# Kernel tuning notes

Hardware: AMD Instinct MI355X
Metric: run time of the kernel (lower is better)

The kernel has to match this reference:

```python
import jax, jax.numpy as jnp
import numpy as np

N_WIRES = 9
N_QRAM_LAYERS = 3
N_QCLS_LAYERS = 5

X = jnp.array([[0, 1], [1, 0]], dtype=jnp.complex64)
CNOT = jnp.array([[1, 0, 0, 0], [0, 1, 0, 0], [0, 0, 0, 1], [0, 0, 1, 0]], dtype=jnp.complex64)


def _rx(t):
    c = jnp.cos(t / 2)
    s = jnp.sin(t / 2)
    # works for scalar t -> (2,2) or batched t [B] -> (B,2,2)
    return jnp.stack([jnp.stack([c + 0j, -1j * s], -1), jnp.stack([-1j * s, c + 0j], -1)], -2)


def _ry(t):
    c = jnp.cos(t / 2)
    s = jnp.sin(t / 2)
    return jnp.stack([jnp.stack([c, -s], -1), jnp.stack([s, c], -1)], -2).astype(jnp.complex64)


def _rz(t):
    e = jnp.exp(-0.5j * t)
    f = jnp.exp(0.5j * t)
    z = jnp.zeros_like(e)
    return jnp.stack([jnp.stack([e, z], -1), jnp.stack([z, f], -1)], -2)


def _rot(phi, theta, omega):
    # PennyLane Rot(phi, theta, omega) = RZ(omega) @ RY(theta) @ RZ(phi)
    return _rz(omega) @ _ry(theta) @ _rz(phi)


def _crz(t):
    e = jnp.exp(-0.5j * t)
    f = jnp.exp(0.5j * t)
    one = jnp.ones((), e.dtype)
    return jnp.diag(jnp.stack([one, one, e, f]))


def _crx(t):
    return jnp.eye(4, dtype=jnp.complex64).at[2:, 2:].set(_rx(t))


def apply_1q(state, U, w):
    # state: [B] + (2,)*N_WIRES ; wire w -> axis 1+w
    s = jnp.moveaxis(state, 1 + w, -1)
    if U.ndim == 3:  # per-sample gate (embedding)
        s = jnp.einsum('bij,b...j->b...i', U, s)
    else:
        s = jnp.einsum('ij,...j->...i', U, s)
    return jnp.moveaxis(s, -1, 1 + w)


def apply_2q(state, U, c, t):
    s = jnp.moveaxis(state, (1 + c, 1 + t), (-2, -1))
    shp = s.shape
    s = s.reshape(shp[:-2] + (4,))
    s = jnp.einsum('ij,...j->...i', U, s)
    return jnp.moveaxis(s.reshape(shp), (-2, -1), (1 + c, 1 + t))


def embed(state, adds):
    # AngleEmbedding: RX(adds[:, i]) on wire i
    for i in range(N_WIRES):
        state = apply_1q(state, _rx(adds[:, i]), i)
    return state


def entangle_block(state, p):
    # p: [36] = 4 params per wire-pair step
    j = 0
    for i in range(N_WIRES):
        ip = (i + 1) % N_WIRES
        state = apply_1q(state, _ry(p[j]), i)
        state = apply_1q(state, _ry(p[j + 1]), ip)
        state = apply_2q(state, CNOT, i, ip)
        state = apply_2q(state, _crz(p[j + 2]), i, ip)
        state = apply_1q(state, X, ip)
        state = apply_2q(state, _crx(p[j + 3]), i, ip)
        j += 4
    return state


def sel_layer(state, w, r):
    # one StronglyEntanglingLayers layer: Rot on each wire, then CNOT ring of range r
    for i in range(N_WIRES):
        state = apply_1q(state, _rot(w[i, 0], w[i, 1], w[i, 2]), i)
    for i in range(N_WIRES):
        state = apply_2q(state, CNOT, i, (i + r) % N_WIRES)
    return state


def circuit(adds, params, weights, params2):
    B = adds.shape[0]
    state = jnp.zeros((B,) + (2,) * N_WIRES, jnp.complex64)
    state = state.at[(slice(None),) + (0,) * N_WIRES].set(1.0)
    state = embed(state, adds)
    for l in range(N_QRAM_LAYERS):
        state = entangle_block(state, params[l * 36:(l + 1) * 36])
    for l in range(N_QRAM_LAYERS):
        r = (l % (N_WIRES - 1)) + 1  # PennyLane default ranges
        state = sel_layer(state, weights[l], r)
    for l in range(N_QCLS_LAYERS):
        state = entangle_block(state, params2[l * 36:(l + 1) * 36])
    probs = jnp.abs(state) ** 2
    p = probs.reshape(B, 2, -1).sum(-1)  # marginal over wire 0
    return p[:, 0] - p[:, 1]  # <PauliZ(0)>


def setup_inputs() -> dict:
    key = jax.random.key(0)
    k1, k2, k3, k4 = jax.random.split(key, 4)
    B = 8192
    return {
        'adds': jax.random.normal(k1, (B, N_WIRES), dtype=jnp.float32),
        'params': jax.random.normal(k2, (N_QRAM_LAYERS * 36,), dtype=jnp.float32),
        'weights': jax.random.normal(k3, (N_QRAM_LAYERS, N_WIRES, N_QRAM_LAYERS), dtype=jnp.float32),
        'params2': jax.random.normal(k4, (N_QCLS_LAYERS * 36,), dtype=jnp.float32),
    }


def reference(adds, params, weights, params2):
    return circuit(adds, params, weights, params2)
```

## Files before the change

kernel.cpp:

```cpp
#include <hip/hip_runtime.h>

#define NQ 9
#define NS 512
#define M2 1024
#define NSIMB 256

#define COEF_ROT_BASE (72*32)
#define COEF_R3_BASE  (COEF_ROT_BASE + 27*8)
#define COEF_FLOATS   (COEF_R3_BASE + 3*128)

typedef __attribute__((ext_vector_type(8))) short bf16x8;
typedef __attribute__((ext_vector_type(4))) float f32x4;

__device__ inline unsigned short f2bf(float f){
  unsigned int u = __float_as_uint(f);
  u += 0x7fffu + ((u >> 16) & 1u);
  return (unsigned short)(u >> 16);
}


template<int LM>
__device__ inline float lxor(float v){
  if constexpr (LM == 1)
    return __int_as_float(__builtin_amdgcn_mov_dpp(__float_as_int(v), 0xB1, 0xF, 0xF, true));
  else if constexpr (LM == 2)
    return __int_as_float(__builtin_amdgcn_mov_dpp(__float_as_int(v), 0x4E, 0xF, 0xF, true));
  else if constexpr (LM == 3)
    return __int_as_float(__builtin_amdgcn_mov_dpp(__float_as_int(v), 0x1B, 0xF, 0xF, true));
  else if constexpr (LM < 32)
    return __int_as_float(__builtin_amdgcn_ds_swizzle(__float_as_int(v), (LM<<10)|0x1F));
  else
    return __shfl_xor(v, LM);
}

template<int M>
__device__ inline float lx(float v){
  if constexpr ((M & 63) == 0) return v;
  else return lxor<(M & 63)>(v);
}

template<int M>
__device__ inline void getp(const float (&ox)[4], const float (&oy)[4],
                            const float2 (&pv)[4], int r, float& qx, float& qy){
  constexpr int MR = (M >> 6) & 3;
  float vx, vy;
  if constexpr ((M & 0x100) != 0){ vx = pv[r^MR].x; vy = pv[r^MR].y; }
  else                           { vx = ox[r^MR];   vy = oy[r^MR];   }
  qx = lx<M>(vx); qy = lx<M>(vy);
}

__device__ inline void xwave(const float (&ax)[4], const float (&ay)[4],
                             int wvb, int lane, float2* xb, float2 (&pv)[4]){
  #pragma unroll
  for (int r = 0; r < 4; ++r) xb[(wvb*4+r)*64 + lane] = make_float2(ax[r], ay[r]);
  __syncthreads();
  #pragma unroll
  for (int r = 0; r < 4; ++r) pv[r] = xb[((wvb^1)*4+r)*64 + lane];
}

template<int CM,int TM>
__device__ inline void stepQ(float (&ax)[4], float (&ay)[4], int wvb, int lane,
                             float2* xb, const float* g){
  constexpr bool HX = ((CM | TM) & 0x100) != 0;
  float2 pv[4];
  if constexpr (HX) xwave(ax, ay, wvb, lane, xb, pv);
  float ox[4], oy[4];
  #pragma unroll
  for (int r = 0; r < 4; ++r){ ox[r] = ax[r]; oy[r] = ay[r]; }
  #pragma unroll
  for (int r = 0; r < 4; ++r){
    float tx,ty,cx,cy,bx,by;
    getp<TM>(ox, oy, pv, r, tx, ty);
    getp<CM>(ox, oy, pv, r, cx, cy);
    getp<(CM^TM)>(ox, oy, pv, r, bx, by);
    int i = (wvb << 8) | (r << 6) | lane;
    int p = ((i & CM) ? 2 : 0) | ((i & TM) ? 1 : 0);
    float4 hx = *(const float4*)(g + p*4);
    float4 hy = *(const float4*)(g + 16 + p*4);
    ax[r] = hx.x*ox[r]-hy.x*oy[r] + hx.y*tx-hy.y*ty + hx.z*cx-hy.z*cy + hx.w*bx-hy.w*by;
    ay[r] = hx.x*oy[r]+hy.x*ox[r] + hx.y*ty+hy.y*tx + hx.z*cy+hy.z*cx + hx.w*by+hy.w*bx;
  }
}

template<int I = 0>
__device__ inline void ent_blkQ(float (&ax)[4], float (&ay)[4], int wvb, int lane,
                                float2* ebA, float2* ebB, const float* S){
  if constexpr      (I == 0) stepQ<0x100,0x080>(ax, ay, wvb, lane, ebA, S);
  else if constexpr (I == 8) stepQ<0x001,0x100>(ax, ay, wvb, lane, ebB, S + 256);
  else                       stepQ<(0x100>>I),(0x080>>I)>(ax, ay, wvb, lane, ebA, S + I*32);
  if constexpr (I < 8) ent_blkQ<I+1>(ax, ay, wvb, lane, ebA, ebB, S);
}

__device__ inline void rot3Q(float (&ax)[4], float (&ay)[4], int wvb, int lane,
                             float2* xb, const float* Mt){
  float2 pv[4];
  xwave(ax, ay, wvb, lane, xb, pv);
  bool w1 = (wvb != 0);
  float l0x[4],l0y[4],l1x[4],l1y[4];
  #pragma unroll
  for (int r = 0; r < 4; ++r){
    l0x[r] = w1 ? pv[r].x : ax[r];  l0y[r] = w1 ? pv[r].y : ay[r];
    l1x[r] = w1 ? ax[r]   : pv[r].x; l1y[r] = w1 ? ay[r]   : pv[r].y;
  }
  #pragma unroll
  for (int r = 0; r < 4; ++r){
    const float4* row = (const float4*)(Mt + ((wvb<<2)|r)*16);
    float4 m0 = row[0], m1 = row[1], m2 = row[2], m3 = row[3];
    float nx, ny;
    nx  = m0.x*l0x[0]-m0.y*l0y[0];  ny  = m0.x*l0y[0]+m0.y*l0x[0];
    nx += m0.z*l0x[1]-m0.w*l0y[1];  ny += m0.z*l0y[1]+m0.w*l0x[1];
    nx += m1.x*l0x[2]-m1.y*l0y[2];  ny += m1.x*l0y[2]+m1.y*l0x[2];
    nx += m1.z*l0x[3]-m1.w*l0y[3];  ny += m1.z*l0y[3]+m1.w*l0x[3];
    nx += m2.x*l1x[0]-m2.y*l1y[0];  ny += m2.x*l1y[0]+m2.y*l1x[0];
    nx += m2.z*l1x[1]-m2.w*l1y[1];  ny += m2.z*l1y[1]+m2.w*l1x[1];
    nx += m3.x*l1x[2]-m3.y*l1y[2];  ny += m3.x*l1y[2]+m3.y*l1x[2];
    nx += m3.z*l1x[3]-m3.w*l1y[3];  ny += m3.z*l1y[3]+m3.w*l1x[3];
    ax[r] = nx; ay[r] = ny;
  }
}

template<int LM>
__device__ inline void rotQ(float (&ax)[4], float (&ay)[4], int lane, const float* u){
  float4 uu = *(const float4*)(u + ((lane & LM) ? 4 : 0));
  #pragma unroll
  for (int r = 0; r < 4; ++r){
    float px = lxor<LM>(ax[r]), py = lxor<LM>(ay[r]);
    float nx = uu.x*ax[r]-uu.y*ay[r] + uu.z*px-uu.w*py;
    float ny = uu.x*ay[r]+uu.y*ax[r] + uu.z*py+uu.w*px;
    ax[r] = nx; ay[r] = ny;
  }
}

template<int I = 3>
__device__ inline void sel_rotsQ(float (&ax)[4], float (&ay)[4], int lane, const float* ub){
  rotQ<(1<<(8-I))>(ax, ay, lane, ub + I*8);
  if constexpr (I < 8) sel_rotsQ<I+1>(ax, ay, lane, ub);
}

template<int TR>
__device__ inline void cn_wr(float (&ax)[4], float (&ay)[4], int wvb){
  if (wvb){
    #pragma unroll
    for (int r = 0; r < 4; ++r) if (!(r & TR)){
      float t = ax[r]; ax[r] = ax[r|TR]; ax[r|TR] = t;
      t = ay[r]; ay[r] = ay[r|TR]; ay[r|TR] = t;
    }
  }
}
template<int TL>
__device__ inline void cn_wl(float (&ax)[4], float (&ay)[4], int wvb){
  if (wvb){
    #pragma unroll
    for (int r = 0; r < 4; ++r){ ax[r] = lxor<TL>(ax[r]); ay[r] = lxor<TL>(ay[r]); }
  }
}
template<int CR,int TR>
__device__ inline void cn_rr(float (&ax)[4], float (&ay)[4]){
  #pragma unroll
  for (int r = 0; r < 4; ++r) if ((r & CR) && !(r & TR)){
    float t = ax[r]; ax[r] = ax[r|TR]; ax[r|TR] = t;
    t = ay[r]; ay[r] = ay[r|TR]; ay[r|TR] = t;
  }
}
template<int CR,int TL>
__device__ inline void cn_rl(float (&ax)[4], float (&ay)[4]){
  #pragma unroll
  for (int r = 0; r < 4; ++r) if (r & CR){ ax[r] = lxor<TL>(ax[r]); ay[r] = lxor<TL>(ay[r]); }
}
template<int CL,int TR>
__device__ inline void cn_lr(float (&ax)[4], float (&ay)[4], int lane){
  bool c = (lane & CL) != 0;
  #pragma unroll
  for (int r = 0; r < 4; ++r) if (!(r & TR)){
    int rp = r | TR;
    float t0x = ax[r], t0y = ay[r];
    ax[r]  = c ? ax[rp] : t0x;  ay[r]  = c ? ay[rp] : t0y;
    ax[rp] = c ? t0x : ax[rp];  ay[rp] = c ? t0y : ay[rp];
  }
}
template<int CL,int TL>
__device__ inline void cn_ll(float (&ax)[4], float (&ay)[4], int lane){
  bool c = (lane & CL) != 0;
  #pragma unroll
  for (int r = 0; r < 4; ++r){
    float px = lxor<TL>(ax[r]), py = lxor<TL>(ay[r]);
    ax[r] = c ? px : ax[r];  ay[r] = c ? py : ay[r];
  }
}
template<int CL>
__device__ inline void cn_lw(float (&ax)[4], float (&ay)[4], int wvb, int lane, float2* xb){
  float2 pv[4];
  xwave(ax, ay, wvb, lane, xb, pv);
  bool c = (lane & CL) != 0;
  #pragma unroll
  for (int r = 0; r < 4; ++r){ ax[r] = c ? pv[r].x : ax[r]; ay[r] = c ? pv[r].y : ay[r]; }
}

__device__ inline void ring1(float (&ax)[4], float (&ay)[4], int wvb, int lane, float2* xb){
  cn_wr<2>(ax,ay,wvb);
  cn_rr<2,1>(ax,ay);
  cn_rl<1,32>(ax,ay);
  cn_ll<32,16>(ax,ay,lane);
  cn_ll<16,8>(ax,ay,lane);
  cn_ll<8,4>(ax,ay,lane);
  cn_ll<4,2>(ax,ay,lane);
  cn_ll<2,1>(ax,ay,lane);
  cn_lw<1>(ax,ay,wvb,lane,xb);
}
__device__ inline void ring2(float (&ax)[4], float (&ay)[4], int wvb, int lane, float2* xb){
  cn_wr<1>(ax,ay,wvb);
  cn_rl<2,32>(ax,ay);
  cn_rl<1,16>(ax,ay);
  cn_ll<32,8>(ax,ay,lane);
  cn_ll<16,4>(ax,ay,lane);
  cn_ll<8,2>(ax,ay,lane);
  cn_ll<4,1>(ax,ay,lane);
  cn_lw<2>(ax,ay,wvb,lane,xb);
  cn_lr<1,2>(ax,ay,lane);
}
__device__ inline void ring3(float (&ax)[4], float (&ay)[4], int wvb, int lane, float2* xb){
  cn_wl<32>(ax,ay,wvb);
  cn_rl<2,16>(ax,ay);
  cn_rl<1,8>(ax,ay);
  cn_ll<32,4>(ax,ay,lane);
  cn_ll<16,2>(ax,ay,lane);
  cn_ll<8,1>(ax,ay,lane);
  cn_lw<4>(ax,ay,wvb,lane,xb);
  cn_lr<2,2>(ax,ay,lane);
  cn_lr<1,1>(ax,ay,lane);
}

__global__ __launch_bounds__(256) void sim_prep(const float* __restrict__ params,
                                                const float* __restrict__ weights,
                                                const float* __restrict__ params2,
                                                const float* __restrict__ adds,
                                                unsigned short* __restrict__ A2,
                                                unsigned short* __restrict__ cT,
                                                float* __restrict__ out, int B){
  int tid = threadIdx.x;

  if (blockIdx.x >= NSIMB){
    int gid = (blockIdx.x - NSIMB) * 256 + tid;
    int b = gid >> 6;
    int lane = gid & 63;
    if (b < B){
      const float* ab = adds + b * NQ;
      float cw[NQ], sw[NQ];
      #pragma unroll
      for (int w = 0; w < NQ; ++w)
        __sincosf(0.5f * ab[w], &sw[w], &cw[w]);
      float p6 = 1.f;
      #pragma unroll
      for (int w = 0; w < 6; ++w)
        p6 *= ((lane >> (5 - w)) & 1) ? sw[w] : cw[w];
      union { unsigned short u[8]; uint4 v; } pk;
      #pragma unroll
      for (int j = 0; j < 8; ++j){
        float p = p6 * (((j>>2)&1) ? sw[6] : cw[6])
                     * (((j>>1)&1) ? sw[7] : cw[7])
                     * (( j    &1) ? sw[8] : cw[8]);
        pk.u[j] = f2bf(p);
      }
      *(uint4*)(cT + (size_t)b * NS + lane*8) = pk.v;
    }
    if (gid < B) out[gid] = 0.f;
    return;
  }

  __shared__ float2 ebufA[1024];
  __shared__ float2 ebufB[1024];
  __shared__ float scoef[COEF_FLOATS];

  if (tid < 72){
    int blk = tid / 9, I = tid % 9;
    const float* p = (blk < 3) ? params + blk*36 : params2 + (blk-3)*36;
    float s0,c0,s1,c1,s2,c2,s3,c3;
    __sincosf(0.5f*p[4*I+0], &s0, &c0);
    __sincosf(0.5f*p[4*I+1], &s1, &c1);
    __sincosf(0.5f*p[4*I+2], &s2, &c2);
    __sincosf(0.5f*p[4*I+3], &s3, &c3);
    float m[4][4] = {
      { c0*c1, -c0*s1, -s0*c1,  s0*s1},
      { c0*s1,  c0*c1, -s0*s1, -s0*c1},
      { s0*c1, -s0*s1,  c0*c1, -c0*s1},
      { s0*s1,  s0*c1,  c0*s1,  c0*c1}};
    float gx[4][4], gy[4][4];
    #pragma unroll
    for (int q = 0; q < 4; ++q){
      gx[0][q] = m[1][q];  gy[0][q] = 0.f;
      gx[1][q] = m[0][q];  gy[1][q] = 0.f;
      gx[2][q] =  c3*c2*m[2][q] - s3*s2*m[3][q];
      gy[2][q] =  c3*s2*m[2][q] - s3*c2*m[3][q];
      gx[3][q] =  s3*s2*m[2][q] + c3*c2*m[3][q];
      gy[3][q] = -(s3*c2*m[2][q] + c3*s2*m[3][q]);
    }
    float* dst = scoef + tid*32;
    #pragma unroll
    for (int pp = 0; pp < 4; ++pp)
      #pragma unroll
      for (int d = 0; d < 4; ++d){
        dst[pp*4+d]    = gx[pp][pp^d];
        dst[16+pp*4+d] = gy[pp][pp^d];
      }
  } else if (tid < 99){
    int r = tid - 72;
    int l = r / 9, i = r % 9;
    const float* w = weights + l*27 + 3*i;
    float phi = w[0], th = w[1], om = w[2];
    float sT,cT,sA,cA,sB,cB;
    __sincosf(0.5f*th, &sT, &cT);
    __sincosf(0.5f*(phi+om), &sA, &cA);
    __sincosf(0.5f*(om-phi), &sB, &cB);
    float* dst = scoef + COEF_ROT_BASE + r*8;
    dst[0] =  cA*cT;  dst[1] = -sA*cT;
    dst[2] = -cB*sT;  dst[3] =  sB*sT;
    dst[4] =  cA*cT;  dst[5] =  sA*cT;
    dst[6] =  cB*sT;  dst[7] =  sB*sT;
  } else if (tid < 123){
    int idx = tid - 99;
    int l = idx >> 3, p = idx & 7;
    float e0x[3], e0y[3], e1x[3], e1y[3];
    #pragma unroll
    for (int w = 0; w < 3; ++w){
      const float* wp = weights + l*27 + 3*w;
      float phi = wp[0], th = wp[1], om = wp[2];
      float sT,cT,sA,cA,sB,cB;
      __sincosf(0.5f*th, &sT, &cT);
      __sincosf(0.5f*(phi+om), &sA, &cA);
      __sincosf(0.5f*(om-phi), &sB, &cB);
      int pw = (p >> (2 - w)) & 1;
      if (pw == 0){ e0x[w] =  cA*cT; e0y[w] = -sA*cT; e1x[w] = -cB*sT; e1y[w] =  sB*sT; }
      else        { e0x[w] =  cB*sT; e0y[w] =  sB*sT; e1x[w] =  cA*cT; e1y[w] =  sA*cT; }
    }
    float* dst = scoef + COEF_R3_BASE + l*128 + p*16;
    #pragma unroll
    for (int q = 0; q < 8; ++q){
      float rx = 1.f, ry = 0.f;
      #pragma unroll
      for (int w = 0; w < 3; ++w){
        int qw = (q >> (2 - w)) & 1;
        float fx = qw ? e1x[w] : e0x[w];
        float fy = qw ? e1y[w] : e0y[w];
        float nx = rx*fx - ry*fy;
        float ny = rx*fy + ry*fx;
        rx = nx; ry = ny;
      }
      dst[q*2]   = rx;
      dst[q*2+1] = ry;
    }
  }
  __syncthreads();

  int wid = tid >> 6, lane = tid & 63;
  int colbit = wid >> 1, wvb = wid & 1;
  int col = blockIdx.x * 2 + colbit;
  float2* ebA = ebufA + colbit * 512;
  float2* ebB = ebufB + colbit * 512;

  float ax[4], ay[4];
  int pc = __popc((unsigned)col) & 3;
  float prx = (pc==0) ? 1.f : (pc==2 ? -1.f : 0.f);
  float pry = (pc==3) ? 1.f : (pc==1 ? -1.f : 0.f);
  #pragma unroll
  for (int r = 0; r < 4; ++r){
    int i = (wvb<<8) | (r<<6) | lane;
    ax[r] = (i == col) ? prx : 0.f;
    ay[r] = (i == col) ? pry : 0.f;
  }

  #pragma unroll 1
  for (int blk = 0; blk < 3; ++blk)
    ent_blkQ<0>(ax, ay, wvb, lane, ebA, ebB, scoef + blk*288);

  rot3Q(ax, ay, wvb, lane, ebA, scoef + COEF_R3_BASE + 0*128);
  sel_rotsQ<3>(ax, ay, lane, scoef + COEF_ROT_BASE + 0*72);
  ring1(ax, ay, wvb, lane, ebB);
  rot3Q(ax, ay, wvb, lane, ebA, scoef + COEF_R3_BASE + 1*128);
  sel_rotsQ<3>(ax, ay, lane, scoef + COEF_ROT_BASE + 1*72);
  ring2(ax, ay, wvb, lane, ebB);
  rot3Q(ax, ay, wvb, lane, ebA, scoef + COEF_R3_BASE + 2*128);
  sel_rotsQ<3>(ax, ay, lane, scoef + COEF_ROT_BASE + 2*72);
  ring3(ax, ay, wvb, lane, ebB);

  #pragma unroll 1
  for (int blk = 3; blk < 8; ++blk)
    ent_blkQ<0>(ax, ay, wvb, lane, ebA, ebB, scoef + blk*288);

  float2* Lb = ebufA;
  #pragma unroll
  for (int r = 0; r < 4; ++r) Lb[(wid*4+r)*64 + lane] = make_float2(ax[r], ay[r]);
  __syncthreads();
  int part = wid >> 1;
  int wb = wid & 1;
  unsigned int* Aw = (unsigned int*)A2;
  #pragma unroll
  for (int r = 0; r < 4; ++r){
    float2 v0 = Lb[(wb*4+r)*64 + lane];
    float2 v1 = Lb[((2+wb)*4+r)*64 + lane];
    float a0 = part ? v0.y : v0.x;
    float a1 = part ? v1.y : v1.x;
    unsigned int pk = (unsigned)f2bf(a0) | ((unsigned)f2bf(a1) << 16);
    int row = (part<<9) + (wb<<8) + (r<<6) + lane;
    Aw[(size_t)blockIdx.x * 1024 + row] = pk;
  }
}

__global__ __launch_bounds__(256) void gemm_out(const unsigned short* __restrict__ A2,
                                                const unsigned short* __restrict__ cT,
                                                float* __restrict__ out){
  int bx = blockIdx.x;
  int by = blockIdx.y;
  int tid = threadIdx.x;
  int wave = tid >> 6, lane = tid & 63;
  int wy = wave >> 1, wx = wave & 1;
  int lane15 = lane & 15, quad = lane >> 4;
  int rowBase = by*128 + wy*64;
  int colBase = bx*128 + wx*64;
  const unsigned int* Aw = (const unsigned int*)A2;
  const short* Bp = (const short*)cT;

  f32x4 acc[4][4];
  #pragma unroll
  for (int i = 0; i < 4; ++i)
    #pragma unroll
    for (int j = 0; j < 4; ++j)
      acc[i][j] = (f32x4){0.f, 0.f, 0.f, 0.f};

  #pragma unroll 4
  for (int k0 = 0; k0 < NS; k0 += 32){
    union { unsigned int w[4]; bf16x8 v; } au[4];
    bf16x8 b[4];
    int kb0 = (k0 >> 1) + (quad << 2);
    #pragma unroll
    for (int mi = 0; mi < 4; ++mi){
      int row = rowBase + mi*16 + lane15;
      #pragma unroll
      for (int d = 0; d < 4; ++d)
        au[mi].w[d] = Aw[(size_t)(kb0 + d)*1024 + row];
    }
    #pragma unroll
    for (int ni = 0; ni < 4; ++ni)
      b[ni] = *(const bf16x8*)(Bp + (size_t)(colBase + ni*16 + lane15)*NS + k0 + quad*8);
    #pragma unroll
    for (int mi = 0; mi < 4; ++mi)
      #pragma unroll
      for (int ni = 0; ni < 4; ++ni)
        acc[mi][ni] = __builtin_amdgcn_mfma_f32_16x16x32_bf16(au[mi].v, b[ni], acc[mi][ni], 0, 0, 0);
  }

  float sign = (by & 2) ? -1.f : 1.f;
  #pragma unroll
  for (int ni = 0; ni < 4; ++ni){
    float cs = 0.f;
    #pragma unroll
    for (int mi = 0; mi < 4; ++mi)
      #pragma unroll
      for (int r = 0; r < 4; ++r)
        cs += acc[mi][ni][r] * acc[mi][ni][r];
    cs += __shfl_xor(cs, 16);
    cs += __shfl_xor(cs, 32);
    if (quad == 0)
      atomicAdd(out + colBase + ni*16 + lane15, sign * cs);
  }
}

extern "C" void kernel_launch(void* const* d_in, const int* in_sizes, int n_in,
                              void* d_out, int out_size, void* d_ws, size_t ws_size,
                              hipStream_t stream) {
  const float* adds    = (const float*)d_in[0];
  const float* params  = (const float*)d_in[1];
  const float* weights = (const float*)d_in[2];
  const float* params2 = (const float*)d_in[3];
  float* out = (float*)d_out;
  int B = in_sizes[0] / NQ;

  unsigned short* A2 = (unsigned short*)d_ws;
  unsigned short* cT = A2 + (size_t)M2 * NS;

  int prepBlocks = (B * 64 + 255) / 256;
  hipLaunchKernelGGL(sim_prep, dim3(NSIMB + prepBlocks), dim3(256), 0, stream,
                     params, weights, params2, adds, A2, cT, out, B);
  hipLaunchKernelGGL(gemm_out, dim3(B / 128, 8), dim3(256), 0, stream, A2, cT, out);
}
```

Before: 111.8 us.

## Simulate one column per 128-thread block and store A in MFMA-ready 8-wide layout

The simulation kernel now runs one basis column per 128-thread block, 512 blocks instead of 256 blocks of 256 threads, which halves shared buffers and drops the transpose-through-LDS epilogue. Each column is written straight into an A layout where 8 consecutive k values per row are contiguous. The GEMM can then load each A fragment as one 16-byte bf16x8 load instead of four strided 32-bit loads. The trade-off is scattered 2-byte global stores in the sim kernel and more, smaller blocks.

After: 130.7 us. 16.9% more time.

```diff
diff --git a/kernel.cpp b/kernel.cpp
--- a/kernel.cpp
+++ b/kernel.cpp
@@ -3,7 +3,7 @@
 #define NQ 9
 #define NS 512
 #define M2 1024
-#define NSIMB 256
+#define NSIMB 512
 
 #define COEF_ROT_BASE (72*32)
 #define COEF_R3_BASE  (COEF_ROT_BASE + 27*8)
@@ -230,7 +230,8 @@
   cn_lr<1,1>(ax,ay,lane);
 }
 
-__global__ __launch_bounds__(256) void sim_prep(const float* __restrict__ params,
+
+__global__ __launch_bounds__(128) void sim_prep(const float* __restrict__ params,
                                                 const float* __restrict__ weights,
                                                 const float* __restrict__ params2,
                                                 const float* __restrict__ adds,
@@ -240,7 +241,7 @@
   int tid = threadIdx.x;
 
   if (blockIdx.x >= NSIMB){
-    int gid = (blockIdx.x - NSIMB) * 256 + tid;
+    int gid = (blockIdx.x - NSIMB) * 128 + tid;
     int b = gid >> 6;
     int lane = gid & 63;
     if (b < B){
@@ -267,8 +268,8 @@
     return;
   }
 
-  __shared__ float2 ebufA[1024];
-  __shared__ float2 ebufB[1024];
+  __shared__ float2 ebufA[512];
+  __shared__ float2 ebufB[512];
   __shared__ float scoef[COEF_FLOATS];
 
   if (tid < 72){
@@ -351,11 +352,8 @@
   }
   __syncthreads();
 
-  int wid = tid >> 6, lane = tid & 63;
-  int colbit = wid >> 1, wvb = wid & 1;
-  int col = blockIdx.x * 2 + colbit;
-  float2* ebA = ebufA + colbit * 512;
-  float2* ebB = ebufB + colbit * 512;
+  int wvb = tid >> 6, lane = tid & 63;
+  int col = blockIdx.x;
 
   float ax[4], ay[4];
   int pc = __popc((unsigned)col) & 3;
@@ -370,38 +368,30 @@
 
   #pragma unroll 1
   for (int blk = 0; blk < 3; ++blk)
-    ent_blkQ<0>(ax, ay, wvb, lane, ebA, ebB, scoef + blk*288);
-
-  rot3Q(ax, ay, wvb, lane, ebA, scoef + COEF_R3_BASE + 0*128);
+    ent_blkQ<0>(ax, ay, wvb, lane, ebufA, ebufB, scoef + blk*288);
+
+  rot3Q(ax, ay, wvb, lane, ebufA, scoef + COEF_R3_BASE + 0*128);
   sel_rotsQ<3>(ax, ay, lane, scoef + COEF_ROT_BASE + 0*72);
-  ring1(ax, ay, wvb, lane, ebB);
-  rot3Q(ax, ay, wvb, lane, ebA, scoef + COEF_R3_BASE + 1*128);
+  ring1(ax, ay, wvb, lane, ebufB);
+  rot3Q(ax, ay, wvb, lane, ebufA, scoef + COEF_R3_BASE + 1*128);
   sel_rotsQ<3>(ax, ay, lane, scoef + COEF_ROT_BASE + 1*72);
-  ring2(ax, ay, wvb, lane, ebB);
-  rot3Q(ax, ay, wvb, lane, ebA, scoef + COEF_R3_BASE + 2*128);
+  ring2(ax, ay, wvb, lane, ebufB);
+  rot3Q(ax, ay, wvb, lane, ebufA, scoef + COEF_R3_BASE + 2*128);
   sel_rotsQ<3>(ax, ay, lane, scoef + COEF_ROT_BASE + 2*72);
-  ring3(ax, ay, wvb, lane, ebB);
+  ring3(ax, ay, wvb, lane, ebufB);
 
   #pragma unroll 1
   for (int blk = 3; blk < 8; ++blk)
-    ent_blkQ<0>(ax, ay, wvb, lane, ebA, ebB, scoef + blk*288);
-
-  float2* Lb = ebufA;
-  #pragma unroll
-  for (int r = 0; r < 4; ++r) Lb[(wid*4+r)*64 + lane] = make_float2(ax[r], ay[r]);
-  __syncthreads();
-  int part = wid >> 1;
-  int wb = wid & 1;
-  unsigned int* Aw = (unsigned int*)A2;
-  #pragma unroll
-  for (int r = 0; r < 4; ++r){
-    float2 v0 = Lb[(wb*4+r)*64 + lane];
-    float2 v1 = Lb[((2+wb)*4+r)*64 + lane];
-    float a0 = part ? v0.y : v0.x;
-    float a1 = part ? v1.y : v1.x;
-    unsigned int pk = (unsigned)f2bf(a0) | ((unsigned)f2bf(a1) << 16);
-    int row = (part<<9) + (wb<<8) + (r<<6) + lane;
-    Aw[(size_t)blockIdx.x * 1024 + row] = pk;
+    ent_blkQ<0>(ax, ay, wvb, lane, ebufA, ebufB, scoef + blk*288);
+
+  int c = col >> 3, d = (col >> 1) & 3, j = col & 1;
+  size_t base = (size_t)c * 1024;
+  int sub = d*2 + j;
+  #pragma unroll
+  for (int r = 0; r < 4; ++r){
+    int i = (wvb<<8) | (r<<6) | lane;
+    A2[(base + i)*8 + sub]       = f2bf(ax[r]);
+    A2[(base + 512 + i)*8 + sub] = f2bf(ay[r]);
   }
 }
 
@@ -416,7 +406,7 @@
   int lane15 = lane & 15, quad = lane >> 4;
   int rowBase = by*128 + wy*64;
   int colBase = bx*128 + wx*64;
-  const unsigned int* Aw = (const unsigned int*)A2;
+  const bf16x8* Ap8 = (const bf16x8*)A2;
   const short* Bp = (const short*)cT;
 
   f32x4 acc[4][4];
@@ -428,16 +418,11 @@
 
   #pragma unroll 4
   for (int k0 = 0; k0 < NS; k0 += 32){
-    union { unsigned int w[4]; bf16x8 v; } au[4];
-    bf16x8 b[4];
-    int kb0 = (k0 >> 1) + (quad << 2);
-    #pragma unroll
-    for (int mi = 0; mi < 4; ++mi){
-      int row = rowBase + mi*16 + lane15;
-      #pragma unroll
-      for (int d = 0; d < 4; ++d)
-        au[mi].w[d] = Aw[(size_t)(kb0 + d)*1024 + row];
-    }
+    bf16x8 a[4], b[4];
+    int c = (k0 >> 3) + quad;
+    #pragma unroll
+    for (int mi = 0; mi < 4; ++mi)
+      a[mi] = Ap8[(size_t)c*1024 + rowBase + mi*16 + lane15];
     #pragma unroll
     for (int ni = 0; ni < 4; ++ni)
       b[ni] = *(const bf16x8*)(Bp + (size_t)(colBase + ni*16 + lane15)*NS + k0 + quad*8);
@@ -445,7 +430,7 @@
     for (int mi = 0; mi < 4; ++mi)
       #pragma unroll
       for (int ni = 0; ni < 4; ++ni)
-        acc[mi][ni] = __builtin_amdgcn_mfma_f32_16x16x32_bf16(au[mi].v, b[ni], acc[mi][ni], 0, 0, 0);
+        acc[mi][ni] = __builtin_amdgcn_mfma_f32_16x16x32_bf16(a[mi], b[ni], acc[mi][ni], 0, 0, 0);
   }
 
   float sign = (by & 2) ? -1.f : 1.f;
@@ -477,8 +462,8 @@
   unsigned short* A2 = (unsigned short*)d_ws;
   unsigned short* cT = A2 + (size_t)M2 * NS;
 
-  int prepBlocks = (B * 64 + 255) / 256;
-  hipLaunchKernelGGL(sim_prep, dim3(NSIMB + prepBlocks), dim3(256), 0, stream,
+  int prepBlocks = (B * 64 + 127) / 128;
+  hipLaunchKernelGGL(sim_prep, dim3(NSIMB + prepBlocks), dim3(128), 0, stream,
                      params, weights, params2, adds, A2, cT, out, B);
   hipLaunchKernelGGL(gemm_out, dim3(B / 128, 8), dim3(256), 0, stream, A2, cT, out);
 }
```
